# Kernel optimization log

Measured on AMD Instinct MI355X. Metric: run time of the kernel, lower is better.

The kernel has to match this reference:

```python
import jax, jax.numpy as jnp
import numpy as np

B, H, W, C = 32, 56, 56, 128
WS, NH, DEPTH = 7, 4, 2
SHIFT = WS // 2
N = WS * WS
HID = 4 * C
CPB = 512


def _layernorm(x, g, b, eps=1e-5):
    m = x.mean(-1, keepdims=True)
    v = ((x - m) ** 2).mean(-1, keepdims=True)
    return (x - m) * jax.lax.rsqrt(v + eps) * g + b


def _window_partition(x):
    b, h, w, c = x.shape
    x = x.reshape(b, h // WS, WS, w // WS, WS, c)
    return x.transpose(0, 1, 3, 2, 4, 5).reshape(-1, N, c)


def _window_reverse(xw, h, w):
    c = xw.shape[-1]
    b = xw.shape[0] // ((h // WS) * (w // WS))
    x = xw.reshape(b, h // WS, w // WS, WS, WS, c)
    return x.transpose(0, 1, 3, 2, 4, 5).reshape(b, h, w, c)


def _rel_index():
    coords = np.stack(np.meshgrid(np.arange(WS), np.arange(WS), indexing='ij'))
    flat = coords.reshape(2, -1)
    rel = (flat[:, :, None] - flat[:, None, :]).transpose(1, 2, 0).astype(np.int64)
    rel[..., 0] += WS - 1
    rel[..., 1] += WS - 1
    rel[..., 0] *= 2 * WS - 1
    return jnp.asarray(rel.sum(-1))  # [N, N]


def _coords_table():
    # SwinV2 log-spaced continuous relative coords table (pretrained_window_size=0 path)
    r = np.arange(-(WS - 1), WS, dtype=np.float32)
    t = np.stack(np.meshgrid(r, r, indexing='ij'), axis=-1)  # [2W-1, 2W-1, 2]
    t = t / (WS - 1) * 8.0
    t = np.sign(t) * np.log2(np.abs(t) + 1.0) / np.log2(8.0)
    return jnp.asarray(t.reshape(-1, 2))  # [(2W-1)^2, 2]


def _shift_mask():
    img = np.zeros((H, W), np.float32)
    cnt = 0
    for hs in (slice(0, -WS), slice(-WS, -SHIFT), slice(-SHIFT, None)):
        for ws_ in (slice(0, -WS), slice(-WS, -SHIFT), slice(-SHIFT, None)):
            img[hs, ws_] = cnt
            cnt += 1
    mw = np.asarray(_window_partition(jnp.asarray(img)[None, :, :, None])).reshape(-1, N)
    diff = mw[:, None, :] - mw[:, :, None]
    return jnp.asarray(np.where(diff != 0, -100.0, 0.0).astype(np.float32))  # [nW, N, N]


def _forward(x, qkv_w, q_bias, v_bias, logit_scale, cpb_w1, cpb_b1, cpb_w2,
             proj_w, proj_b, norm1_g, norm1_b, mlp_w1, mlp_b1, mlp_w2, mlp_b2,
             norm2_g, norm2_b, pm_g, pm_b, pm_w):
    rel_idx = _rel_index()
    table = _coords_table()
    smask = _shift_mask()
    for i in range(DEPTH):
        shift = 0 if i % 2 == 0 else SHIFT
        xs = jnp.roll(x, (-shift, -shift), axis=(1, 2)) if shift else x
        xw = _window_partition(xs)  # [B*nW, N, C]
        bias = jnp.concatenate([q_bias[i], jnp.zeros_like(q_bias[i]), v_bias[i]])
        qkv = (xw @ qkv_w[i] + bias).reshape(-1, N, 3, NH, C // NH).transpose(2, 0, 3, 1, 4)
        q, k, v = qkv[0], qkv[1], qkv[2]  # [B*nW, NH, N, hd]
        qn = q / jnp.maximum(jnp.linalg.norm(q, axis=-1, keepdims=True), 1e-12)
        kn = k / jnp.maximum(jnp.linalg.norm(k, axis=-1, keepdims=True), 1e-12)
        scale = jnp.exp(jnp.minimum(logit_scale[i], jnp.log(100.0)))  # [NH,1,1]
        attn = jnp.einsum('bhnd,bhmd->bhnm', qn, kn) * scale
        rpb = 16.0 * jax.nn.sigmoid(
            (jax.nn.relu(table @ cpb_w1[i] + cpb_b1[i]) @ cpb_w2[i])[rel_idx])  # [N,N,NH]
        attn = attn + rpb.transpose(2, 0, 1)[None]
        if shift:
            nW = smask.shape[0]
            attn = (attn.reshape(-1, nW, NH, N, N) + smask[None, :, None]).reshape(-1, NH, N, N)
        attn = jax.nn.softmax(attn, axis=-1)
        out = jnp.einsum('bhnm,bhmd->bnhd', attn, v).reshape(-1, N, C)
        out = out @ proj_w[i] + proj_b[i]
        xs = _window_reverse(out, H, W)
        if shift:
            xs = jnp.roll(xs, (shift, shift), axis=(1, 2))
        # SwinV2 post-norm residuals
        x = x + _layernorm(xs, norm1_g[i], norm1_b[i])
        y = jax.nn.gelu(x @ mlp_w1[i] + mlp_b1[i], approximate=False) @ mlp_w2[i] + mlp_b2[i]
        x = x + _layernorm(y, norm2_g[i], norm2_b[i])
    # PatchMerging: [B,H,W,C] -> [B,H/2,W/2,4C] -> norm -> Linear(4C,2C)
    xm = x.reshape(B, H // 2, 2, W // 2, 2, C).transpose(0, 1, 3, 2, 4, 5)
    xm = xm.reshape(B, H // 2, W // 2, 4 * C)
    return _layernorm(xm, pm_g, pm_b) @ pm_w


def setup_inputs() -> dict:
    key = jax.random.key(0)
    ks = jax.random.split(key, 8)
    s = 0.02
    rn = lambda k, shp: jax.random.normal(k, shp, jnp.float32) * s
    return dict(
        x=jax.random.normal(ks[0], (B, H, W, C), jnp.float32),
        qkv_w=rn(ks[1], (DEPTH, C, 3 * C)),
        q_bias=jnp.zeros((DEPTH, C), jnp.float32),
        v_bias=jnp.zeros((DEPTH, C), jnp.float32),
        logit_scale=jnp.full((DEPTH, NH, 1, 1), np.log(10.0), jnp.float32),
        cpb_w1=rn(ks[2], (DEPTH, 2, CPB)),
        cpb_b1=jnp.zeros((DEPTH, CPB), jnp.float32),
        cpb_w2=rn(ks[3], (DEPTH, CPB, NH)),
        proj_w=rn(ks[4], (DEPTH, C, C)),
        proj_b=jnp.zeros((DEPTH, C), jnp.float32),
        norm1_g=jnp.ones((DEPTH, C), jnp.float32),
        norm1_b=jnp.zeros((DEPTH, C), jnp.float32),
        mlp_w1=rn(ks[5], (DEPTH, C, HID)),
        mlp_b1=jnp.zeros((DEPTH, HID), jnp.float32),
        mlp_w2=rn(ks[6], (DEPTH, HID, C)),
        mlp_b2=jnp.zeros((DEPTH, C), jnp.float32),
        norm2_g=jnp.ones((DEPTH, C), jnp.float32),
        norm2_b=jnp.zeros((DEPTH, C), jnp.float32),
        pm_g=jnp.ones((4 * C,), jnp.float32),
        pm_b=jnp.zeros((4 * C,), jnp.float32),
        pm_w=rn(ks[7], (4 * C, 2 * C)),
    )


def reference(x, qkv_w, q_bias, v_bias, logit_scale, cpb_w1, cpb_b1, cpb_w2,
              proj_w, proj_b, norm1_g, norm1_b, mlp_w1, mlp_b1, mlp_w2, mlp_b2,
              norm2_g, norm2_b, pm_g, pm_b, pm_w):
    return _forward(x, qkv_w, q_bias, v_bias, logit_scale, cpb_w1, cpb_b1, cpb_w2,
                    proj_w, proj_b, norm1_g, norm1_b, mlp_w1, mlp_b1, mlp_w2, mlp_b2,
                    norm2_g, norm2_b, pm_g, pm_b, pm_w)
```

## Files before the change

### kernel.cpp

```cpp
#include <hip/hip_runtime.h>
#include <math.h>


namespace {
constexpr int kTok = 32 * 56 * 56;
}

typedef __attribute__((ext_vector_type(8))) short bf16x8;
typedef __attribute__((ext_vector_type(4))) float f32x4;

union FragU {
    int4 i4;
    bf16x8 b8;
    unsigned short u[8];
};

__device__ __forceinline__ short f2bf(float f) {
    unsigned u = __float_as_uint(f);
    return (short)((u + 0x7FFFu + ((u >> 16) & 1u)) >> 16);
}
__device__ __forceinline__ float bf2f(unsigned short u) {
    return __uint_as_float(((unsigned)u) << 16);
}
__device__ __forceinline__ unsigned cvt_pk_bf16(float a, float b) {
    unsigned r;
    asm("v_cvt_pk_bf16_f32 %0, %1, %2" : "=v"(r) : "v"(a), "v"(b));
    return r;
}
__device__ __forceinline__ float gelu_t(float x) {
    float x2 = x * x;
    float t0 = fmaf(0.044715f * x2, x, x);
    float e = exp2f(2.3022227f * t0);
    float r = __builtin_amdgcn_rcpf(e + 1.0f);
    return fmaf(-x, r, x);
}

__global__ __launch_bounds__(256) void k_cpb(
    const float* __restrict__ w1, const float* __restrict__ b1,
    const float* __restrict__ w2, float* __restrict__ out169) {
    int t = blockIdx.x;
    int ia = t / 13, ib = t % 13;
    float r0 = (float)(ia - 6) * (8.0f / 6.0f);
    float s0 = (r0 > 0.f) ? 1.f : (r0 < 0.f ? -1.f : 0.f);
    float t0 = s0 * log2f(fabsf(r0) + 1.0f) * (1.0f / 3.0f);
    float r1 = (float)(ib - 6) * (8.0f / 6.0f);
    float s1 = (r1 > 0.f) ? 1.f : (r1 < 0.f ? -1.f : 0.f);
    float t1 = s1 * log2f(fabsf(r1) + 1.0f) * (1.0f / 3.0f);

    int tid = threadIdx.x;
    float p0 = 0, p1 = 0, p2 = 0, p3 = 0;
    for (int c = tid; c < 512; c += 256) {
        float hv = fmaxf(t0 * w1[c] + t1 * w1[512 + c] + b1[c], 0.0f);
        p0 += hv * w2[c * 4 + 0];
        p1 += hv * w2[c * 4 + 1];
        p2 += hv * w2[c * 4 + 2];
        p3 += hv * w2[c * 4 + 3];
    }
    __shared__ float red[256][4];
    red[tid][0] = p0; red[tid][1] = p1; red[tid][2] = p2; red[tid][3] = p3;
    __syncthreads();
    for (int s = 128; s > 0; s >>= 1) {
        if (tid < s) {
            red[tid][0] += red[tid + s][0];
            red[tid][1] += red[tid + s][1];
            red[tid][2] += red[tid + s][2];
            red[tid][3] += red[tid + s][3];
        }
        __syncthreads();
    }
    if (tid < 4) out169[t * 4 + tid] = red[0][tid];
}

__global__ void k_rpb(const float* __restrict__ out169, float* __restrict__ rpb64) {
    int e = blockIdx.x * 256 + threadIdx.x;
    if (e >= 4 * 64 * 64) return;
    int h = e >> 12, r = e & 4095;
    int i = r >> 6, j = r & 63;
    float val;
    if (j >= 49) {
        val = -30000.0f;
    } else if (i >= 49) {
        val = 0.0f;
    } else {
        int dp = i / 7 - j / 7 + 6;
        int dq = i % 7 - j % 7 + 6;
        float v = out169[(dp * 13 + dq) * 4 + h];
        val = 16.0f / (1.0f + expf(-v));
    }
    rpb64[e] = val;
}

__global__ __launch_bounds__(256) void k_cvtw(
    const float* __restrict__ W, short* __restrict__ Wb, int Kb, int N) {
    int slt = blockIdx.x * 256 + threadIdx.x;
    if (slt >= Kb * N) return;
    int nn = slt & 63;
    int tmp = slt >> 6;
    int kb = tmp % Kb;
    int nt = tmp / Kb;
    int n = nt * 64 + nn;
    int k0 = kb * 8;
    union { int4 i4; short s8[8]; } u;
#pragma unroll
    for (int e = 0; e < 8; ++e) u.s8[e] = f2bf(W[(size_t)(k0 + e) * N + n]);
    int nns = (nn & ~3) | ((nn ^ kb) & 3);
    *(int4*)(Wb + (((size_t)tmp) * 64 + nns) * 8) = u.i4;
}

__global__ __launch_bounds__(256) void k_cvtx(
    const float* __restrict__ x, short* __restrict__ xb) {
    size_t e = ((size_t)blockIdx.x * 256 + threadIdx.x) * 8;
    const float* src = x + e;
    float4 f0 = *(const float4*)src;
    float4 f1 = *(const float4*)(src + 4);
    union { int4 i4; short s8[8]; } u;
    u.s8[0] = f2bf(f0.x); u.s8[1] = f2bf(f0.y);
    u.s8[2] = f2bf(f0.z); u.s8[3] = f2bf(f0.w);
    u.s8[4] = f2bf(f1.x); u.s8[5] = f2bf(f1.y);
    u.s8[6] = f2bf(f1.z); u.s8[7] = f2bf(f1.w);
    *(int4*)(xb + e) = u.i4;
}

template <int K, int EPI, int NT>
__global__ __launch_bounds__(256) void k_gemm(
    const short* __restrict__ Ain, const short* __restrict__ Wb,
    const float* __restrict__ bias0, const float* __restrict__ bias1,
    void* __restrict__ Out, int ostride, int shift) {
    constexpr int Kb = K / 8;
    constexpr int NC = K / 128;
    __shared__ int4 As4[2048];
    __shared__ int4 Ws4[1024];
    int tid = threadIdx.x;
    int nwg = gridDim.x;
    int chunk = nwg >> 3;
    int lid = (blockIdx.x & 7) * chunk + (blockIdx.x >> 3);
    int mt = lid / NT, nt = lid - mt * NT;
    int mb = mt * 128;
    int w = tid >> 6, l = tid & 63, lr = l & 15, lg = l >> 4;
    const f32x4 fz = {0.f, 0.f, 0.f, 0.f};
    f32x4 acc[2][4];
#pragma unroll
    for (int mi = 0; mi < 2; ++mi)
#pragma unroll
        for (int ni = 0; ni < 4; ++ni) acc[mi][ni] = fz;

    for (int c = 0; c < NC; ++c) {
        if (c) __syncthreads();
#pragma unroll
        for (int it = 0; it < 8; ++it) {
            int s = it * 256 + tid;
            int m = s >> 4, kb = s & 15;
            int gm = mb + m;
            if (EPI == 1 && shift) {
                int b = gm / 3136, r = gm % 3136;
                int hh = r / 56 + shift; if (hh >= 56) hh -= 56;
                int ww = r % 56 + shift; if (ww >= 56) ww -= 56;
                gm = b * 3136 + hh * 56 + ww;
            }
            int slot = kb * 128 + ((m & ~7) | ((m ^ kb) & 7));
            As4[slot] = *(const int4*)(Ain + (size_t)gm * K + c * 128 + kb * 8);
        }
        {
            const int4* wsrc = (const int4*)(Wb + ((size_t)nt * Kb + c * 16) * 64 * 8);
#pragma unroll
            for (int it = 0; it < 4; ++it) Ws4[it * 256 + tid] = wsrc[it * 256 + tid];
        }
        __syncthreads();
#pragma unroll
        for (int kk = 0; kk < 4; ++kk) {
            int kbl = kk * 4 + lg;
            int m0 = w * 32 + lr;
            bf16x8 a0 = *(const bf16x8*)&As4[kbl * 128 + ((m0 & ~7) | ((m0 ^ kbl) & 7))];
            int m1 = m0 + 16;
            bf16x8 a1 = *(const bf16x8*)&As4[kbl * 128 + ((m1 & ~7) | ((m1 ^ kbl) & 7))];
#pragma unroll
            for (int ni = 0; ni < 4; ++ni) {
                int nn = lr + 16 * ni;
                bf16x8 bfr = *(const bf16x8*)&Ws4[kbl * 64 + ((nn & ~3) | ((nn ^ kbl) & 3))];
                acc[0][ni] = __builtin_amdgcn_mfma_f32_16x16x32_bf16(a0, bfr, acc[0][ni], 0, 0, 0);
                acc[1][ni] = __builtin_amdgcn_mfma_f32_16x16x32_bf16(a1, bfr, acc[1][ni], 0, 0, 0);
            }
        }
    }
#pragma unroll
    for (int ni = 0; ni < 4; ++ni) {
        int col = nt * 64 + ni * 16 + lr;
        float bv = 0.f;
        if (EPI == 1) bv = (col < 128) ? bias0[col] : ((col < 256) ? 0.f : bias1[col - 256]);
#pragma unroll
        for (int mi = 0; mi < 2; ++mi) {
#pragma unroll
            for (int r = 0; r < 4; ++r) {
                int row = mb + w * 32 + mi * 16 + lg * 4 + r;
                float v = acc[mi][ni][r] + bv;
                if (EPI == 0) {
                    ((float*)Out)[(size_t)row * ostride + col] = v;
                } else {
                    ((short*)Out)[(size_t)row * 384 + col] = f2bf(v);
                }
            }
        }
    }
}

template <int K, bool RF32>
__global__ __launch_bounds__(256) void k_gemm_ln(
    const short* __restrict__ Ain, const short* __restrict__ Wb,
    const float* __restrict__ bias, const float* __restrict__ g,
    const float* __restrict__ bt, const void* __restrict__ resid,
    short* __restrict__ xoutb, int shift) {
    constexpr int Kb = K / 8;
    constexpr int NC = K / 128;
    __shared__ int4 As4[1024];
    __shared__ int4 Ws4[2048];
    int tid = threadIdx.x;
    int mb = blockIdx.x * 64;
    int w = tid >> 6, l = tid & 63, lr = l & 15, lg = l >> 4;
    const f32x4 fz = {0.f, 0.f, 0.f, 0.f};
    f32x4 acc[8];
#pragma unroll
    for (int ni = 0; ni < 8; ++ni) acc[ni] = fz;

    for (int c = 0; c < NC; ++c) {
        if (c) __syncthreads();
#pragma unroll
        for (int it = 0; it < 4; ++it) {
            int s = it * 256 + tid;
            int m = s >> 4, kb = s & 15;
            int slot = kb * 64 + ((m & ~7) | ((m ^ kb) & 7));
            As4[slot] = *(const int4*)(Ain + (size_t)(mb + m) * K + c * 128 + kb * 8);
        }
        {
            const int4* w0 = (const int4*)(Wb + ((size_t)(c * 16)) * 64 * 8);
            const int4* w1 = (const int4*)(Wb + ((size_t)(Kb + c * 16)) * 64 * 8);
#pragma unroll
            for (int it = 0; it < 4; ++it) {
                Ws4[it * 256 + tid] = w0[it * 256 + tid];
                Ws4[1024 + it * 256 + tid] = w1[it * 256 + tid];
            }
        }
        __syncthreads();
#pragma unroll
        for (int kk = 0; kk < 4; ++kk) {
            int kbl = kk * 4 + lg;
            int m0 = w * 16 + lr;
            bf16x8 a0 = *(const bf16x8*)&As4[kbl * 64 + ((m0 & ~7) | ((m0 ^ kbl) & 7))];
#pragma unroll
            for (int ni = 0; ni < 8; ++ni) {
                int nn = lr + 16 * (ni & 3);
                bf16x8 bfr = *(const bf16x8*)&Ws4[(ni >> 2) * 1024 + kbl * 64 +
                                                  ((nn & ~3) | ((nn ^ kbl) & 3))];
                acc[ni] = __builtin_amdgcn_mfma_f32_16x16x32_bf16(a0, bfr, acc[ni], 0, 0, 0);
            }
        }
    }
    float bv[8], gv[8], btv[8];
#pragma unroll
    for (int ni = 0; ni < 8; ++ni) {
        int col = ni * 16 + lr;
        bv[ni] = bias[col]; gv[ni] = g[col]; btv[ni] = bt[col];
    }
#pragma unroll
    for (int r = 0; r < 4; ++r) {
        int row = mb + w * 16 + lg * 4 + r;
        float v[8];
        float s1 = 0.f, s2 = 0.f;
#pragma unroll
        for (int ni = 0; ni < 8; ++ni) {
            v[ni] = acc[ni][r] + bv[ni];
            s1 += v[ni];
            s2 = fmaf(v[ni], v[ni], s2);
        }
#pragma unroll
        for (int off = 8; off >= 1; off >>= 1) {
            s1 += __shfl_xor(s1, off);
            s2 += __shfl_xor(s2, off);
        }
        float mean = s1 * (1.0f / 128.0f);
        float var = s2 * (1.0f / 128.0f) - mean * mean;
        float rstd = rsqrtf(var + 1e-5f);
        int mo = row;
        if (shift) {
            int b = row / 3136, rr = row % 3136;
            int hh = rr / 56 + shift; if (hh >= 56) hh -= 56;
            int ww = rr % 56 + shift; if (ww >= 56) ww -= 56;
            mo = b * 3136 + hh * 56 + ww;
        }
        size_t base = (size_t)mo * 128;
#pragma unroll
        for (int ni = 0; ni < 8; ++ni) {
            int col = ni * 16 + lr;
            float rv = RF32 ? ((const float*)resid)[base + col]
                            : bf2f(((const unsigned short*)resid)[base + col]);
            float o = rv + (v[ni] - mean) * rstd * gv[ni] + btv[ni];
            xoutb[base + col] = f2bf(o);
        }
    }
}

__global__ __launch_bounds__(256) void k_mlp(
    short* __restrict__ xb, const short* __restrict__ W1b,
    const short* __restrict__ W2b, const float* __restrict__ b1,
    const float* __restrict__ b2, const float* __restrict__ g,
    const float* __restrict__ bt) {
    __shared__ int4 W1s[1024];
    __shared__ int4 W2s[1024];
    __shared__ short Hs[4 * 2304];
    int tid = threadIdx.x;
    int mb = blockIdx.x * 128;
    int w = tid >> 6, l = tid & 63, lr = l & 15, lg = l >> 4;
    const f32x4 fz = {0.f, 0.f, 0.f, 0.f};
    short* Hw = Hs + w * 2304;

    int4 xfrag[2][4];
#pragma unroll
    for (int mi = 0; mi < 2; ++mi)
#pragma unroll
        for (int kk = 0; kk < 4; ++kk)
            xfrag[mi][kk] = *(const int4*)(
                xb + (size_t)(mb + w * 32 + mi * 16 + lr) * 128 + kk * 32 + lg * 8);

    f32x4 acc2[2][8];
#pragma unroll
    for (int mi = 0; mi < 2; ++mi)
#pragma unroll
        for (int ni = 0; ni < 8; ++ni) acc2[mi][ni] = fz;

    for (int c = 0; c < 8; ++c) {
        __syncthreads();
        {
            const int4* w1src = (const int4*)(W1b + (size_t)c * 8192);
#pragma unroll
            for (int it = 0; it < 4; ++it) W1s[it * 256 + tid] = w1src[it * 256 + tid];
            const int4* w2a = (const int4*)(W2b + (size_t)(c * 8) * 512);
            const int4* w2c = (const int4*)(W2b + (size_t)(64 + c * 8) * 512);
#pragma unroll
            for (int it = 0; it < 2; ++it) {
                W2s[it * 256 + tid] = w2a[it * 256 + tid];
                W2s[512 + it * 256 + tid] = w2c[it * 256 + tid];
            }
        }
        __syncthreads();
        f32x4 a1[2][4];
#pragma unroll
        for (int mi = 0; mi < 2; ++mi)
#pragma unroll
            for (int ct = 0; ct < 4; ++ct) a1[mi][ct] = fz;
        __builtin_amdgcn_s_setprio(1);
#pragma unroll
        for (int kk = 0; kk < 4; ++kk) {
            int kbl = kk * 4 + lg;
            FragU xa0; xa0.i4 = xfrag[0][kk];
            FragU xa1; xa1.i4 = xfrag[1][kk];
#pragma unroll
            for (int ct = 0; ct < 4; ++ct) {
                int nn = lr + 16 * ct;
                bf16x8 w1f = *(const bf16x8*)&W1s[kbl * 64 + ((nn & ~3) | ((nn ^ kbl) & 3))];
                a1[0][ct] = __builtin_amdgcn_mfma_f32_16x16x32_bf16(w1f, xa0.b8, a1[0][ct], 0, 0, 0);
                a1[1][ct] = __builtin_amdgcn_mfma_f32_16x16x32_bf16(w1f, xa1.b8, a1[1][ct], 0, 0, 0);
            }
        }
        __builtin_amdgcn_s_setprio(0);
#pragma unroll
        for (int mi = 0; mi < 2; ++mi) {
#pragma unroll
            for (int ct = 0; ct < 4; ++ct) {
                float4 bb = *(const float4*)(b1 + c * 64 + ct * 16 + lg * 4);
                float h0 = gelu_t(a1[mi][ct][0] + bb.x);
                float h1 = gelu_t(a1[mi][ct][1] + bb.y);
                float h2 = gelu_t(a1[mi][ct][2] + bb.z);
                float h3 = gelu_t(a1[mi][ct][3] + bb.w);
                unsigned p0 = cvt_pk_bf16(h0, h1);
                unsigned p1 = cvt_pk_bf16(h2, h3);
                *(int2*)&Hw[(mi * 16 + lr) * 72 + ct * 16 + lg * 4] =
                    make_int2((int)p0, (int)p1);
            }
        }
        __builtin_amdgcn_s_setprio(1);
#pragma unroll
        for (int kc = 0; kc < 2; ++kc) {
            int kbl = kc * 4 + lg;
            FragU ha0; ha0.i4 = *(const int4*)&Hw[lr * 72 + kc * 32 + lg * 8];
            FragU ha1; ha1.i4 = *(const int4*)&Hw[(16 + lr) * 72 + kc * 32 + lg * 8];
#pragma unroll
            for (int ni = 0; ni < 8; ++ni) {
                int nn = lr + 16 * (ni & 3);
                bf16x8 w2f = *(const bf16x8*)&W2s[(ni >> 2) * 512 + kbl * 64 +
                                                  ((nn & ~3) | ((nn ^ kbl) & 3))];
                acc2[0][ni] = __builtin_amdgcn_mfma_f32_16x16x32_bf16(ha0.b8, w2f, acc2[0][ni], 0, 0, 0);
                acc2[1][ni] = __builtin_amdgcn_mfma_f32_16x16x32_bf16(ha1.b8, w2f, acc2[1][ni], 0, 0, 0);
            }
        }
        __builtin_amdgcn_s_setprio(0);
    }

    float bv[8], gv[8], btv[8];
#pragma unroll
    for (int ni = 0; ni < 8; ++ni) {
        int col = ni * 16 + lr;
        bv[ni] = b2[col]; gv[ni] = g[col]; btv[ni] = bt[col];
    }
#pragma unroll
    for (int mi = 0; mi < 2; ++mi) {
#pragma unroll
        for (int r = 0; r < 4; ++r) {
            int row = mb + w * 32 + mi * 16 + lg * 4 + r;
            float v[8];
            float s1 = 0.f, s2 = 0.f;
#pragma unroll
            for (int ni = 0; ni < 8; ++ni) {
                v[ni] = acc2[mi][ni][r] + bv[ni];
                s1 += v[ni];
                s2 = fmaf(v[ni], v[ni], s2);
            }
#pragma unroll
            for (int off = 8; off >= 1; off >>= 1) {
                s1 += __shfl_xor(s1, off);
                s2 += __shfl_xor(s2, off);
            }
            float mean = s1 * (1.0f / 128.0f);
            float var = s2 * (1.0f / 128.0f) - mean * mean;
            float rstd = rsqrtf(var + 1e-5f);
            size_t base = (size_t)row * 128;
#pragma unroll
            for (int ni = 0; ni < 8; ++ni) {
                int col = ni * 16 + lr;
                float rv = bf2f(((const unsigned short*)xb)[base + col]);
                float o = rv + (v[ni] - mean) * rstd * gv[ni] + btv[ni];
                xb[base + col] = f2bf(o);
            }
        }
    }
}

__global__ __launch_bounds__(256) void k_attn(
    const short* __restrict__ qkv, const float* __restrict__ rpb64,
    const float* __restrict__ ls, short* __restrict__ aout, int shift) {
    __shared__ short lds[4 * 3584];
    int wid = blockIdx.x;
    int b = wid >> 6, wrem = wid & 63;
    int wh = wrem >> 3, ww_ = wrem & 7;
    int h = threadIdx.x >> 6;
    int l = threadIdx.x & 63, lr = l & 15, lg = l >> 4;
    short* Pt = lds + h * 3584;
    short* Vt = Pt + 1152;
    float* invks = (float*)(Vt + 2304);
    int tokbase = b * 3136 + wh * 7 * 56 + ww_ * 7;

    float scale = __expf(fminf(ls[h], 4.6051702f));
    int4 qf[4], kf[4], vf[4];
    const int4 zero4 = make_int4(0, 0, 0, 0);
#pragma unroll
    for (int t = 0; t < 4; ++t) {
        int i = t * 16 + lr;
        bool valid = (i < 49);
        int tok = tokbase + (i / 7) * 56 + (i % 7);
        const short* base = qkv + (size_t)tok * 384 + h * 32 + lg * 8;
        qf[t] = valid ? *(const int4*)base : zero4;
        kf[t] = valid ? *(const int4*)(base + 128) : zero4;
    }
#pragma unroll
    for (int t = 0; t < 4; ++t) {
        int e = t * 64 + l;
        int j = e >> 2, dq = e & 3;
        if (j < 49) {
            int tok = tokbase + (j / 7) * 56 + (j % 7);
            vf[t] = *(const int4*)(qkv + (size_t)tok * 384 + 256 + h * 32 + dq * 8);
        } else {
            vf[t] = zero4;
        }
    }

    float invq[4];
#pragma unroll
    for (int t = 0; t < 4; ++t) {
        {
            FragU u; u.i4 = qf[t];
            float ss = 0.f;
#pragma unroll
            for (int e = 0; e < 8; ++e) { float x = bf2f(u.u[e]); ss = fmaf(x, x, ss); }
            ss += __shfl_xor(ss, 16);
            ss += __shfl_xor(ss, 32);
            invq[t] = scale / fmaxf(sqrtf(ss), 1e-12f);
        }
        {
            FragU u; u.i4 = kf[t];
            float ss = 0.f;
#pragma unroll
            for (int e = 0; e < 8; ++e) { float x = bf2f(u.u[e]); ss = fmaf(x, x, ss); }
            ss += __shfl_xor(ss, 16);
            ss += __shfl_xor(ss, 32);
            float ik = 1.0f / fmaxf(sqrtf(ss), 1e-12f);
            if (l < 16) invks[t * 16 + l] = ik;
        }
    }

    for (int t = l; t < 480; t += 64) {
        Vt[(t / 15) * 72 + 49 + (t % 15)] = 0;
    }
#pragma unroll
    for (int t = 0; t < 4; ++t) {
        int e = t * 64 + l;
        int j = e >> 2, dq = e & 3;
        if (j < 49) {
            FragU u; u.i4 = vf[t];
#pragma unroll
            for (int ee = 0; ee < 8; ++ee) Vt[(dq * 8 + ee) * 72 + j] = (short)u.u[ee];
        }
    }

    float ika[4][4];
#pragma unroll
    for (int jt = 0; jt < 4; ++jt) {
        float4 v4 = *(const float4*)&invks[jt * 16 + lg * 4];
        ika[jt][0] = v4.x; ika[jt][1] = v4.y; ika[jt][2] = v4.z; ika[jt][3] = v4.w;
    }

    bool edge = (shift != 0) && ((wh == 7) || (ww_ == 7));
    const float* rbase = rpb64 + h * 4096;
    const f32x4 fz = {0.f, 0.f, 0.f, 0.f};
    f32x4 oacc[2][4];
#pragma unroll
    for (int mi = 0; mi < 2; ++mi)
#pragma unroll
        for (int ni = 0; ni < 4; ++ni) oacc[mi][ni] = fz;

#pragma unroll
    for (int qt = 0; qt < 4; ++qt) {
        f32x4 at[4];
        __builtin_amdgcn_s_setprio(1);
#pragma unroll
        for (int jt = 0; jt < 4; ++jt) {
            FragU a; a.i4 = kf[jt];
            FragU bq; bq.i4 = qf[qt];
            at[jt] = __builtin_amdgcn_mfma_f32_16x16x32_bf16(a.b8, bq.b8, fz, 0, 0, 0);
        }
        __builtin_amdgcn_s_setprio(0);

        float iq = invq[qt];
        int qi = qt * 16 + lr;
        int qc = (qi < 49) ? qi : 48;
        int rlq = 0, clq = 0;
        if (edge) {
            rlq = (wh == 7) ? ((qc / 7) < 4 ? 1 : 2) : 0;
            clq = (ww_ == 7) ? ((qc % 7) < 4 ? 1 : 2) : 0;
        }
#pragma unroll
        for (int jt = 0; jt < 4; ++jt) {
            float4 rv = *(const float4*)(rbase + qc * 64 + jt * 16 + lg * 4);
            float rr[4] = {rv.x, rv.y, rv.z, rv.w};
#pragma unroll
            for (int r = 0; r < 4; ++r) {
                float v = fmaf(at[jt][r] * ika[jt][r], iq, rr[r]);
                if (edge) {
                    int j = jt * 16 + lg * 4 + r;
                    int jc = (j < 49) ? j : 48;
                    int rlk = (wh == 7) ? ((jc / 7) < 4 ? 1 : 2) : 0;
                    int clk = (ww_ == 7) ? ((jc % 7) < 4 ? 1 : 2) : 0;
                    if (rlk != rlq || clk != clq) v -= 100.0f;
                }
                at[jt][r] = v;
            }
        }
        float m = -1e30f;
#pragma unroll
        for (int jt = 0; jt < 4; ++jt)
#pragma unroll
            for (int r = 0; r < 4; ++r) m = fmaxf(m, at[jt][r]);
        m = fmaxf(m, __shfl_xor(m, 16));
        m = fmaxf(m, __shfl_xor(m, 32));
        float s = 0.f;
#pragma unroll
        for (int jt = 0; jt < 4; ++jt)
#pragma unroll
            for (int r = 0; r < 4; ++r) {
                float p = __expf(at[jt][r] - m);
                at[jt][r] = p;
                s += p;
            }
        s += __shfl_xor(s, 16);
        s += __shfl_xor(s, 32);
        float inv = 1.0f / s;
#pragma unroll
        for (int jt = 0; jt < 4; ++jt) {
            unsigned lo = cvt_pk_bf16(at[jt][0] * inv, at[jt][1] * inv);
            unsigned hi = cvt_pk_bf16(at[jt][2] * inv, at[jt][3] * inv);
            *(int2*)&Pt[lr * 72 + jt * 16 + lg * 4] = make_int2((int)lo, (int)hi);
        }
        __builtin_amdgcn_s_setprio(1);
#pragma unroll
        for (int kc = 0; kc < 2; ++kc) {
            FragU pb;
            pb.i4 = *(const int4*)&Pt[lr * 72 + kc * 32 + lg * 8];
#pragma unroll
            for (int mi = 0; mi < 2; ++mi) {
                FragU va;
                va.i4 = *(const int4*)&Vt[(mi * 16 + lr) * 72 + kc * 32 + lg * 8];
                oacc[mi][qt] = __builtin_amdgcn_mfma_f32_16x16x32_bf16(
                    va.b8, pb.b8, oacc[mi][qt], 0, 0, 0);
            }
        }
        __builtin_amdgcn_s_setprio(0);
    }

#pragma unroll
    for (int ni = 0; ni < 4; ++ni) {
        int qrow = ni * 16 + lr;
        if (qrow < 49) {
            int tok = tokbase + (qrow / 7) * 56 + (qrow % 7);
#pragma unroll
            for (int mi = 0; mi < 2; ++mi) {
                unsigned lo = cvt_pk_bf16(oacc[mi][ni][0], oacc[mi][ni][1]);
                unsigned hi = cvt_pk_bf16(oacc[mi][ni][2], oacc[mi][ni][3]);
                *(int2*)&aout[(size_t)tok * 128 + h * 32 + mi * 16 + lg * 4] =
                    make_int2((int)lo, (int)hi);
            }
        }
    }
}

__global__ __launch_bounds__(256) void k_pmln(
    const short* __restrict__ x, const float* __restrict__ g,
    const float* __restrict__ bt, short* __restrict__ outb) {
    int m2 = blockIdx.x * 4 + (threadIdx.x >> 6);
    int l = threadIdx.x & 63;
    int b = m2 / 784, r = m2 % 784;
    int h2 = r / 28, w2 = r % 28;
    int q0 = l * 8;
    int i2 = q0 >> 8, j2 = (q0 >> 7) & 1, c = q0 & 127;
    const short* src = x + (size_t)((b * 56 + 2 * h2 + i2) * 56 + 2 * w2 + j2) * 128 + c;
    FragU u; u.i4 = *(const int4*)src;
    float v[8];
#pragma unroll
    for (int e = 0; e < 8; ++e) v[e] = bf2f(u.u[e]);
    float s1 = 0.f, s2 = 0.f;
#pragma unroll
    for (int e = 0; e < 8; ++e) { s1 += v[e]; s2 = fmaf(v[e], v[e], s2); }
#pragma unroll
    for (int off = 32; off >= 1; off >>= 1) {
        s1 += __shfl_xor(s1, off);
        s2 += __shfl_xor(s2, off);
    }
    float mean = s1 * (1.0f / 512.0f);
    float var = s2 * (1.0f / 512.0f) - mean * mean;
    float rstd = rsqrtf(var + 1e-5f);
    union { int4 i4; short s8[8]; } o;
#pragma unroll
    for (int e = 0; e < 8; ++e)
        o.s8[e] = f2bf((v[e] - mean) * rstd * g[q0 + e] + bt[q0 + e]);
    *(int4*)(outb + (size_t)m2 * 512 + q0) = o.i4;
}

extern "C" void kernel_launch(void* const* d_in, const int* in_sizes, int n_in,
                              void* d_out, int out_size, void* d_ws, size_t ws_size,
                              hipStream_t stream) {
    const float* x_in   = (const float*)d_in[0];
    const float* qkv_w  = (const float*)d_in[1];
    const float* q_bias = (const float*)d_in[2];
    const float* v_bias = (const float*)d_in[3];
    const float* lscale = (const float*)d_in[4];
    const float* cpb_w1 = (const float*)d_in[5];
    const float* cpb_b1 = (const float*)d_in[6];
    const float* cpb_w2 = (const float*)d_in[7];
    const float* proj_w = (const float*)d_in[8];
    const float* proj_b = (const float*)d_in[9];
    const float* n1g    = (const float*)d_in[10];
    const float* n1b    = (const float*)d_in[11];
    const float* mw1    = (const float*)d_in[12];
    const float* mb1    = (const float*)d_in[13];
    const float* mw2    = (const float*)d_in[14];
    const float* mb2    = (const float*)d_in[15];
    const float* n2g    = (const float*)d_in[16];
    const float* n2b    = (const float*)d_in[17];
    const float* pmg    = (const float*)d_in[18];
    const float* pmb    = (const float*)d_in[19];
    const float* pmw    = (const float*)d_in[20];
    float* out = (float*)d_out;

    float* wsf     = (float*)d_ws;
    float* R1      = wsf + (size_t)12845056;
    short* qkvb    = (short*)R1;
    short* attnout = (short*)(R1 + (size_t)19267584);
    short* pmin    = (short*)R1;
    short* xb      = (short*)(R1 + (size_t)25690112);
    float* wtail   = R1 + (size_t)38535168;
    short* wqkvb   = (short*)wtail;
    short* wprojb  = wqkvb + 49152;
    short* wm1b    = wprojb + 16384;
    short* wm2b    = wm1b + 65536;
    short* wpmb    = wm2b + 65536;
    float* out169  = wtail + 163840;
    float* rpb64   = out169 + 704;

    k_cvtx<<<6272, 256, 0, stream>>>(x_in, xb);

    for (int i = 0; i < 2; ++i) {
        int shift = i ? 3 : 0;
        k_cpb<<<169, 256, 0, stream>>>(cpb_w1 + i * 1024, cpb_b1 + i * 512,
                                       cpb_w2 + i * 2048, out169);
        k_rpb<<<64, 256, 0, stream>>>(out169, rpb64);
        k_cvtw<<<24, 256, 0, stream>>>(qkv_w + i * 49152, wqkvb, 16, 384);
        k_cvtw<<<8, 256, 0, stream>>>(proj_w + i * 16384, wprojb, 16, 128);
        k_cvtw<<<32, 256, 0, stream>>>(mw1 + i * 65536, wm1b, 16, 512);
        k_cvtw<<<32, 256, 0, stream>>>(mw2 + i * 65536, wm2b, 64, 128);

        k_gemm<128, 1, 6><<<4704, 256, 0, stream>>>(
            xb, wqkvb, q_bias + i * 128, v_bias + i * 128, qkvb, 384, shift);
        k_attn<<<2048, 256, 0, stream>>>(
            qkvb, rpb64, lscale + i * 4, attnout, shift);
        if (i == 0) {
            k_gemm_ln<128, true><<<1568, 256, 0, stream>>>(
                attnout, wprojb, proj_b, n1g, n1b, x_in, xb, shift);
        } else {
            k_gemm_ln<128, false><<<1568, 256, 0, stream>>>(
                attnout, wprojb, proj_b + i * 128, n1g + i * 128, n1b + i * 128,
                xb, xb, shift);
        }
        k_mlp<<<784, 256, 0, stream>>>(
            xb, wm1b, wm2b, mb1 + i * 512, mb2 + i * 128,
            n2g + i * 128, n2b + i * 128);
    }
    k_cvtw<<<64, 256, 0, stream>>>(pmw, wpmb, 64, 256);
    k_pmln<<<6272, 256, 0, stream>>>(xb, pmg, pmb, pmin);
    k_gemm<512, 0, 4><<<784, 256, 0, stream>>>(
        pmin, wpmb, nullptr, nullptr, out, 256, 0);
}
```

Before: 395.8 us.

## Batch weight conversion and bias prep into single launches, prefetch MLP weights into registers

Replaces the eleven small per-layer weight-conversion, CPB and RPB launches with one combined conversion kernel plus one CPB and one RPB kernel covering both layers. The goal is to cut launch count and serialization gaps on the stream. In the MLP kernel, the next chunk's weights are now loaded into registers while the current chunk's MFMAs run, then stored to shared memory, overlapping global load latency with compute. The trade-off is higher register pressure, and the converted weights move to the start of the workspace.

```diff
diff --git a/kernel.cpp b/kernel.cpp
--- a/kernel.cpp
+++ b/kernel.cpp
@@ -38,7 +38,12 @@
 __global__ __launch_bounds__(256) void k_cpb(
     const float* __restrict__ w1, const float* __restrict__ b1,
     const float* __restrict__ w2, float* __restrict__ out169) {
-    int t = blockIdx.x;
+    int L = blockIdx.x / 169;
+    int t = blockIdx.x % 169;
+    const float* w1L = w1 + L * 1024;
+    const float* b1L = b1 + L * 512;
+    const float* w2L = w2 + L * 2048;
+    float* outL = out169 + L * 704;
     int ia = t / 13, ib = t % 13;
     float r0 = (float)(ia - 6) * (8.0f / 6.0f);
     float s0 = (r0 > 0.f) ? 1.f : (r0 < 0.f ? -1.f : 0.f);
@@ -50,11 +55,11 @@
     int tid = threadIdx.x;
     float p0 = 0, p1 = 0, p2 = 0, p3 = 0;
     for (int c = tid; c < 512; c += 256) {
-        float hv = fmaxf(t0 * w1[c] + t1 * w1[512 + c] + b1[c], 0.0f);
-        p0 += hv * w2[c * 4 + 0];
-        p1 += hv * w2[c * 4 + 1];
-        p2 += hv * w2[c * 4 + 2];
-        p3 += hv * w2[c * 4 + 3];
+        float hv = fmaxf(t0 * w1L[c] + t1 * w1L[512 + c] + b1L[c], 0.0f);
+        p0 += hv * w2L[c * 4 + 0];
+        p1 += hv * w2L[c * 4 + 1];
+        p2 += hv * w2L[c * 4 + 2];
+        p3 += hv * w2L[c * 4 + 3];
     }
     __shared__ float red[256][4];
     red[tid][0] = p0; red[tid][1] = p1; red[tid][2] = p2; red[tid][3] = p3;
@@ -68,12 +73,12 @@
         }
         __syncthreads();
     }
-    if (tid < 4) out169[t * 4 + tid] = red[0][tid];
+    if (tid < 4) outL[t * 4 + tid] = red[0][tid];
 }
 
 __global__ void k_rpb(const float* __restrict__ out169, float* __restrict__ rpb64) {
-    int e = blockIdx.x * 256 + threadIdx.x;
-    if (e >= 4 * 64 * 64) return;
+    int e2 = blockIdx.x * 256 + threadIdx.x;
+    int L = e2 >> 14, e = e2 & 16383;
     int h = e >> 12, r = e & 4095;
     int i = r >> 6, j = r & 63;
     float val;
@@ -84,16 +89,14 @@
     } else {
         int dp = i / 7 - j / 7 + 6;
         int dq = i % 7 - j % 7 + 6;
-        float v = out169[(dp * 13 + dq) * 4 + h];
+        float v = out169[L * 704 + (dp * 13 + dq) * 4 + h];
         val = 16.0f / (1.0f + expf(-v));
     }
-    rpb64[e] = val;
-}
-
-__global__ __launch_bounds__(256) void k_cvtw(
-    const float* __restrict__ W, short* __restrict__ Wb, int Kb, int N) {
-    int slt = blockIdx.x * 256 + threadIdx.x;
-    if (slt >= Kb * N) return;
+    rpb64[e2] = val;
+}
+
+__device__ __forceinline__ void cvt_slot(
+    const float* __restrict__ W, short* __restrict__ Wb, int slt, int Kb, int N) {
     int nn = slt & 63;
     int tmp = slt >> 6;
     int kb = tmp % Kb;
@@ -105,6 +108,36 @@
     for (int e = 0; e < 8; ++e) u.s8[e] = f2bf(W[(size_t)(k0 + e) * N + n]);
     int nns = (nn & ~3) | ((nn ^ kb) & 3);
     *(int4*)(Wb + (((size_t)tmp) * 64 + nns) * 8) = u.i4;
+}
+
+__global__ __launch_bounds__(256) void k_cvtall(
+    const float* __restrict__ qkv_w, const float* __restrict__ proj_w,
+    const float* __restrict__ mw1, const float* __restrict__ mw2,
+    const float* __restrict__ pmw, short* __restrict__ wall) {
+    int s = blockIdx.x * 256 + threadIdx.x;
+    short* wqkvb  = wall;
+    short* wprojb = wall + 98304;
+    short* wm1b   = wall + 131072;
+    short* wm2b   = wall + 262144;
+    short* wpmb   = wall + 393216;
+    if (s < 12288) {
+        int L = s / 6144, r = s % 6144;
+        cvt_slot(qkv_w + L * 49152, wqkvb + L * 49152, r, 16, 384);
+    } else if (s < 16384) {
+        int s2 = s - 12288;
+        int L = s2 / 2048, r = s2 % 2048;
+        cvt_slot(proj_w + L * 16384, wprojb + L * 16384, r, 16, 128);
+    } else if (s < 32768) {
+        int s2 = s - 16384;
+        int L = s2 / 8192, r = s2 % 8192;
+        cvt_slot(mw1 + L * 65536, wm1b + L * 65536, r, 16, 512);
+    } else if (s < 49152) {
+        int s2 = s - 32768;
+        int L = s2 / 8192, r = s2 % 8192;
+        cvt_slot(mw2 + L * 65536, wm2b + L * 65536, r, 64, 128);
+    } else {
+        cvt_slot(pmw, wpmb, s - 49152, 64, 256);
+    }
 }
 
 __global__ __launch_bounds__(256) void k_cvtx(
@@ -326,21 +359,31 @@
 #pragma unroll
         for (int ni = 0; ni < 8; ++ni) acc2[mi][ni] = fz;
 
+    int4 wr0, wr1, wr2, wr3, wr4, wr5, wr6, wr7;
+#define LOADW(c)                                                            \
+    {                                                                       \
+        const int4* w1src = (const int4*)(W1b + (size_t)(c) * 8192);        \
+        wr0 = w1src[tid]; wr1 = w1src[256 + tid];                           \
+        wr2 = w1src[512 + tid]; wr3 = w1src[768 + tid];                     \
+        const int4* w2a = (const int4*)(W2b + (size_t)((c) * 8) * 512);     \
+        const int4* w2c = (const int4*)(W2b + (size_t)(64 + (c) * 8) * 512);\
+        wr4 = w2a[tid]; wr5 = w2a[256 + tid];                               \
+        wr6 = w2c[tid]; wr7 = w2c[256 + tid];                               \
+    }
+#define STOREW()                                                            \
+    {                                                                       \
+        W1s[tid] = wr0; W1s[256 + tid] = wr1;                               \
+        W1s[512 + tid] = wr2; W1s[768 + tid] = wr3;                         \
+        W2s[tid] = wr4; W2s[256 + tid] = wr5;                               \
+        W2s[512 + tid] = wr6; W2s[768 + tid] = wr7;                         \
+    }
+
+    LOADW(0);
+    STOREW();
+    __syncthreads();
+
     for (int c = 0; c < 8; ++c) {
-        __syncthreads();
-        {
-            const int4* w1src = (const int4*)(W1b + (size_t)c * 8192);
-#pragma unroll
-            for (int it = 0; it < 4; ++it) W1s[it * 256 + tid] = w1src[it * 256 + tid];
-            const int4* w2a = (const int4*)(W2b + (size_t)(c * 8) * 512);
-            const int4* w2c = (const int4*)(W2b + (size_t)(64 + c * 8) * 512);
-#pragma unroll
-            for (int it = 0; it < 2; ++it) {
-                W2s[it * 256 + tid] = w2a[it * 256 + tid];
-                W2s[512 + it * 256 + tid] = w2c[it * 256 + tid];
-            }
-        }
-        __syncthreads();
+        if (c < 7) LOADW(c + 1);
         f32x4 a1[2][4];
 #pragma unroll
         for (int mi = 0; mi < 2; ++mi)
@@ -392,7 +435,14 @@
             }
         }
         __builtin_amdgcn_s_setprio(0);
-    }
+        if (c < 7) {
+            __syncthreads();
+            STOREW();
+            __syncthreads();
+        }
+    }
+#undef LOADW
+#undef STOREW
 
     float bv[8], gv[8], btv[8];
 #pragma unroll
@@ -677,50 +727,46 @@
     const float* pmw    = (const float*)d_in[20];
     float* out = (float*)d_out;
 
-    float* wsf     = (float*)d_ws;
+    float* wsf    = (float*)d_ws;
+    short* wall   = (short*)wsf;
+    short* wqkvb  = wall;
+    short* wprojb = wall + 98304;
+    short* wm1b   = wall + 131072;
+    short* wm2b   = wall + 262144;
+    short* wpmb   = wall + 393216;
+    float* out169 = wsf + 262144;
+    float* rpb64  = out169 + 1408;
+
     float* R1      = wsf + (size_t)12845056;
     short* qkvb    = (short*)R1;
     short* attnout = (short*)(R1 + (size_t)19267584);
     short* pmin    = (short*)R1;
     short* xb      = (short*)(R1 + (size_t)25690112);
-    float* wtail   = R1 + (size_t)38535168;
-    short* wqkvb   = (short*)wtail;
-    short* wprojb  = wqkvb + 49152;
-    short* wm1b    = wprojb + 16384;
-    short* wm2b    = wm1b + 65536;
-    short* wpmb    = wm2b + 65536;
-    float* out169  = wtail + 163840;
-    float* rpb64   = out169 + 704;
-
+
+    k_cvtall<<<256, 256, 0, stream>>>(qkv_w, proj_w, mw1, mw2, pmw, wall);
+    k_cpb<<<338, 256, 0, stream>>>(cpb_w1, cpb_b1, cpb_w2, out169);
+    k_rpb<<<128, 256, 0, stream>>>(out169, rpb64);
     k_cvtx<<<6272, 256, 0, stream>>>(x_in, xb);
 
     for (int i = 0; i < 2; ++i) {
         int shift = i ? 3 : 0;
-        k_cpb<<<169, 256, 0, stream>>>(cpb_w1 + i * 1024, cpb_b1 + i * 512,
-                                       cpb_w2 + i * 2048, out169);
-        k_rpb<<<64, 256, 0, stream>>>(out169, rpb64);
-        k_cvtw<<<24, 256, 0, stream>>>(qkv_w + i * 49152, wqkvb, 16, 384);
-        k_cvtw<<<8, 256, 0, stream>>>(proj_w + i * 16384, wprojb, 16, 128);
-        k_cvtw<<<32, 256, 0, stream>>>(mw1 + i * 65536, wm1b, 16, 512);
-        k_cvtw<<<32, 256, 0, stream>>>(mw2 + i * 65536, wm2b, 64, 128);
-
         k_gemm<128, 1, 6><<<4704, 256, 0, stream>>>(
-            xb, wqkvb, q_bias + i * 128, v_bias + i * 128, qkvb, 384, shift);
+            xb, wqkvb + i * 49152, q_bias + i * 128, v_bias + i * 128,
+            qkvb, 384, shift);
         k_attn<<<2048, 256, 0, stream>>>(
-            qkvb, rpb64, lscale + i * 4, attnout, shift);
+            qkvb, rpb64 + i * 16384, lscale + i * 4, attnout, shift);
         if (i == 0) {
             k_gemm_ln<128, true><<<1568, 256, 0, stream>>>(
                 attnout, wprojb, proj_b, n1g, n1b, x_in, xb, shift);
         } else {
             k_gemm_ln<128, false><<<1568, 256, 0, stream>>>(
-                attnout, wprojb, proj_b + i * 128, n1g + i * 128, n1b + i * 128,
+                attnout, wprojb + 16384, proj_b + 128, n1g + 128, n1b + 128,
                 xb, xb, shift);
         }
         k_mlp<<<784, 256, 0, stream>>>(
-            xb, wm1b, wm2b, mb1 + i * 512, mb2 + i * 128,
-            n2g + i * 128, n2b + i * 128);
-    }
-    k_cvtw<<<64, 256, 0, stream>>>(pmw, wpmb, 64, 256);
+            xb, wm1b + i * 65536, wm2b + i * 65536, mb1 + i * 512,
+            mb2 + i * 128, n2g + i * 128, n2b + i * 128);
+    }
     k_pmln<<<6272, 256, 0, stream>>>(xb, pmg, pmb, pmin);
     k_gemm<512, 0, 4><<<784, 256, 0, stream>>>(
         pmin, wpmb, nullptr, nullptr, out, 256, 0);
```

New measurement: 380.4 us. -3.9%, faster.
